# Kernel optimization log

Measured on AMD Instinct MI355X. Metric: run time of the kernel, lower is better.

Reference implementation:

```python
import jax, jax.numpy as jnp
import numpy as np

D_MODEL = 1024
NUM_HEADS = 16
HEAD_DIM = D_MODEL // NUM_HEADS
ROPE_BASE = 10000.0


def _rope_cos_sin(seq_len, head_dim, dtype):
    # inv_freq over half the head dim (standard 1D RoPE)
    inv_freq = 1.0 / (ROPE_BASE ** (jnp.arange(0, head_dim, 2, dtype=jnp.float32) / head_dim))
    ang = jnp.arange(seq_len, dtype=jnp.float32)[:, None] * inv_freq[None, :]  # [S, hd/2]
    cos = jnp.concatenate([jnp.cos(ang), jnp.cos(ang)], axis=-1).astype(dtype)  # [S, hd]
    sin = jnp.concatenate([jnp.sin(ang), jnp.sin(ang)], axis=-1).astype(dtype)
    return cos, sin


def _rotate_half(t):
    t1, t2 = jnp.split(t, 2, axis=-1)
    return jnp.concatenate([-t2, t1], axis=-1)


def _apply_rope(t, cos, sin):
    # t: [B, H, S, hd]; cos/sin: [S, hd]
    return t * cos[None, None, :, :] + _rotate_half(t) * sin[None, None, :, :]


def setup_inputs() -> dict:
    key = jax.random.key(0)
    k1, k2, k3 = jax.random.split(key, 3)
    B, S = 2, 2048
    x = jax.random.normal(k1, (B, S, D_MODEL), dtype=jnp.float32)
    w_qkv = jax.random.normal(k2, (D_MODEL, 3 * D_MODEL), dtype=jnp.float32) * (D_MODEL ** -0.5)
    w_proj = jax.random.normal(k3, (D_MODEL, D_MODEL), dtype=jnp.float32) * (D_MODEL ** -0.5)
    b_proj = jnp.zeros((D_MODEL,), dtype=jnp.float32)
    return {"x": x, "w_qkv": w_qkv, "w_proj": w_proj, "b_proj": b_proj, "causal": 1}


def reference(x, w_qkv, w_proj, b_proj, causal):
    B, S, D = x.shape
    scale = HEAD_DIM ** -0.5
    qkv = x @ w_qkv  # [B, S, 3D]
    q, k, v = jnp.split(qkv, 3, axis=-1)

    def to_heads(t):
        return t.reshape(B, S, NUM_HEADS, HEAD_DIM).transpose(0, 2, 1, 3)  # [B,H,S,hd]

    q, k, v = to_heads(q), to_heads(k), to_heads(v)

    cos, sin = _rope_cos_sin(S, HEAD_DIM, x.dtype)
    q = _apply_rope(q, cos, sin)
    k = _apply_rope(k, cos, sin)

    attn = jnp.einsum('bhqd,bhkd->bhqk', q, k) * scale  # [B,H,S,S]
    if causal:
        causal_mask = jnp.triu(jnp.ones((S, S), dtype=bool), k=1)
        attn = jnp.where(causal_mask[None, None, :, :], jnp.float32(-jnp.inf).astype(attn.dtype), attn)
    attn = jax.nn.softmax(attn, axis=-1)
    out = jnp.einsum('bhqk,bhkd->bhqd', attn, v)  # [B,H,S,hd]
    out = out.transpose(0, 2, 1, 3).reshape(B, S, D)
    return out @ w_proj + b_proj
```

## Files before the change

kernel.cpp:

```cpp
#include <hip/hip_runtime.h>
#include <stdint.h>
#include <math.h>

#define B_   2
#define S_   2048
#define D_   1024
#define H_   16
#define HD_  64
#define M_   (B_*S_)
#define N3_  (3*D_)

typedef __bf16 bf16;
typedef __bf16 bf16x2 __attribute__((ext_vector_type(2)));
typedef __bf16 bf16x4v __attribute__((ext_vector_type(4)));
typedef __bf16 bf16x8 __attribute__((ext_vector_type(8)));
typedef float  f32x4 __attribute__((ext_vector_type(4)));
typedef float  f32x16 __attribute__((ext_vector_type(16)));

__device__ __forceinline__ void gload_lds16(const void* g, void* l) {
  __builtin_amdgcn_global_load_lds(
      (__attribute__((address_space(1))) const unsigned int*)g,
      (__attribute__((address_space(3))) unsigned int*)l, 16, 0, 0);
}

__global__ __launch_bounds__(256) void prep_kernel(const float* __restrict__ x, bf16* __restrict__ xb,
                                                   const float* __restrict__ w_qkv, bf16* __restrict__ wqkvT,
                                                   const float* __restrict__ w_proj, bf16* __restrict__ wprojT,
                                                   float* __restrict__ cosT, float* __restrict__ sinT) {
  __shared__ float tile[32][33];
  int blk = blockIdx.x, tid = threadIdx.x;
  if (blk < 1024) {
#pragma unroll
    for (int it = 0; it < 4; it++) {
      int i = (blk * 4 + it) * 256 + tid;
      float4 v = ((const float4*)x)[i];
      bf16x4v o;
      o[0] = (bf16)v.x; o[1] = (bf16)v.y; o[2] = (bf16)v.z; o[3] = (bf16)v.w;
      *(bf16x4v*)(xb + (size_t)i * 4) = o;
    }
  } else if (blk < 5120) {
    const float* in; bf16* out; int R, C, tb;
    if (blk < 4096) { in = w_qkv;  out = wqkvT;  R = 1024; C = 3072; tb = blk - 1024; }
    else            { in = w_proj; out = wprojT; R = 1024; C = 1024; tb = blk - 4096; }
    int nbx = C >> 5;
    int bx = tb % nbx, by = tb / nbx;
    int c0 = bx * 32, r0 = by * 32;
    int tx = tid & 31, ty = tid >> 5;
#pragma unroll
    for (int j = 0; j < 4; j++)
      tile[ty + j * 8][tx] = in[(size_t)(r0 + ty + j * 8) * C + c0 + tx];
    __syncthreads();
#pragma unroll
    for (int j = 0; j < 4; j++)
      out[(size_t)(c0 + ty + j * 8) * R + r0 + tx] = (bf16)tile[tx][ty + j * 8];
  } else {
    int i = (blk - 5120) * 256 + tid;
    int s = i >> 5, d = i & 31;
    float inv = powf(10000.0f, -(float)d * (1.0f / 32.0f));
    float a = (float)s * inv;
    float sv, cv;
    sincosf(a, &sv, &cv);
    cosT[i] = cv; sinT[i] = sv;
  }
}

__global__ __launch_bounds__(256) void gemm128(const bf16* __restrict__ A,
                                               const bf16* __restrict__ Bt,
                                               int M, int N, int K,
                                               bf16* __restrict__ Cb,
                                               const float* __restrict__ cosT,
                                               const float* __restrict__ sinT,
                                               bf16* __restrict__ vt) {
  __shared__ bf16 As[128 * 32];
  __shared__ bf16 Bs[128 * 32];
  int tid = threadIdx.x;
  int lane = tid & 63, w = tid >> 6;
  int nwg = gridDim.x * gridDim.y;
  int bid = blockIdx.y * gridDim.x + blockIdx.x;
  int sw = (bid & 7) * (nwg >> 3) + (bid >> 3);
  int bx = sw % gridDim.x, by = sw / gridDim.x;
  int m0 = by * 128, n0 = bx * 128;
  int m_off = (w >> 1) * 64, n_off = (w & 1) * 64;
  f32x4 acc[4][4] = {};

  const char* Ab = (const char*)A;
  const char* Bb = (const char*)Bt;
  int srow = (lane >> 2);
  int skb  = (lane & 3) * 16;

  for (int k0 = 0; k0 < K; k0 += 32) {
    for (int j = 0; j < 2; j++) {
      int seg = j * 4 + w;
      int row = seg * 16 + srow;
      gload_lds16(Ab + ((size_t)(m0 + row) * K + k0) * 2 + skb, (char*)As + seg * 1024);
      gload_lds16(Bb + ((size_t)(n0 + row) * K + k0) * 2 + skb, (char*)Bs + seg * 1024);
    }
    __syncthreads();
    int rl = lane & 15;
    int kgb = (lane >> 4) * 16;
    bf16x8 a[4], b[4];
    for (int i = 0; i < 4; i++)
      a[i] = *(const bf16x8*)((const char*)As + (m_off + i * 16 + rl) * 64 + kgb);
    for (int i = 0; i < 4; i++)
      b[i] = *(const bf16x8*)((const char*)Bs + (n_off + i * 16 + rl) * 64 + kgb);
    for (int i = 0; i < 4; i++)
      for (int j = 0; j < 4; j++)
        acc[i][j] = __builtin_amdgcn_mfma_f32_16x16x32_bf16(a[i], b[j], acc[i][j], 0, 0, 0);
    __syncthreads();
  }

  int rq = (lane >> 4) * 4, cl = lane & 15;
  if ((n0 + n_off) < 2048) {
    for (int i = 0; i < 4; i++)
      for (int r = 0; r < 4; r++) {
        int row = m0 + m_off + i * 16 + rq + r;
        int srw = row & 2047;
        for (int j = 0; j < 2; j++) {
          int d2 = j * 16 + cl;
          float c = cosT[srw * 32 + d2], sn = sinT[srw * 32 + d2];
          float x1 = acc[i][j][r], x2 = acc[i][j + 2][r];
          Cb[(size_t)row * N + n0 + n_off + d2]      = (bf16)(x1 * c - x2 * sn);
          Cb[(size_t)row * N + n0 + n_off + d2 + 32] = (bf16)(x2 * c + x1 * sn);
        }
      }
  } else {
    int posbase = ((rq & 4) << 1) | ((rq & 8) >> 1);
    for (int i = 0; i < 4; i++) {
      int row0 = m0 + m_off + i * 16;
      int b = row0 >> 11;
      int sbase = (row0 & 2047) + posbase;
      for (int j = 0; j < 4; j++) {
        int col = n0 + n_off + j * 16 + cl - 2048;
        bf16x4v pv;
        pv[0] = (bf16)acc[i][j][0]; pv[1] = (bf16)acc[i][j][1];
        pv[2] = (bf16)acc[i][j][2]; pv[3] = (bf16)acc[i][j][3];
        *(bf16x4v*)(vt + ((size_t)(b * 1024 + col)) * 2048 + sbase) = pv;
      }
    }
  }
}

__global__ __launch_bounds__(256) void gemm_proj(const bf16* __restrict__ A,
                                                 const bf16* __restrict__ Bt,
                                                 float* __restrict__ Cf,
                                                 const float* __restrict__ bias) {
  __shared__ bf16 As[64 * 32];
  __shared__ bf16 Bs[128 * 32];
  const int K = 1024, N = 1024;
  int tid = threadIdx.x;
  int lane = tid & 63, w = tid >> 6;
  int bid = blockIdx.y * gridDim.x + blockIdx.x;
  int sw = (bid & 7) * 64 + (bid >> 3);
  int bx = sw & 7, by = sw >> 3;
  int m0 = by * 64, n0 = bx * 128;
  int m_off = (w >> 1) * 32, n_off = (w & 1) * 64;
  f32x4 acc[2][4] = {};

  const char* Ab = (const char*)A;
  const char* Bb = (const char*)Bt;
  int arow = tid >> 2, achk = (tid & 3) * 16;

  for (int k0 = 0; k0 < K; k0 += 32) {
    gload_lds16(Ab + ((size_t)(m0 + arow) * K + k0) * 2 + achk, (char*)As + tid * 16);
    gload_lds16(Bb + ((size_t)(n0 + arow) * K + k0) * 2 + achk, (char*)Bs + tid * 16);
    gload_lds16(Bb + ((size_t)(n0 + 64 + arow) * K + k0) * 2 + achk, (char*)Bs + 4096 + tid * 16);
    __syncthreads();
    int rl = lane & 15;
    int kgb = (lane >> 4) * 16;
    bf16x8 a[2], b[4];
    for (int i = 0; i < 2; i++)
      a[i] = *(const bf16x8*)((const char*)As + (m_off + i * 16 + rl) * 64 + kgb);
    for (int j = 0; j < 4; j++)
      b[j] = *(const bf16x8*)((const char*)Bs + (n_off + j * 16 + rl) * 64 + kgb);
    for (int i = 0; i < 2; i++)
      for (int j = 0; j < 4; j++)
        acc[i][j] = __builtin_amdgcn_mfma_f32_16x16x32_bf16(a[i], b[j], acc[i][j], 0, 0, 0);
    __syncthreads();
  }

  int rq = (lane >> 4) * 4, cl = lane & 15;
  for (int i = 0; i < 2; i++)
    for (int j = 0; j < 4; j++) {
      int col = n0 + n_off + j * 16 + cl;
      float bv = bias[col];
      for (int r = 0; r < 4; r++) {
        int row = m0 + m_off + i * 16 + rq + r;
        Cf[(size_t)row * N + col] = acc[i][j][r] + bv;
      }
    }
}

__global__ __launch_bounds__(512, 4) void attn_kernel(const bf16* __restrict__ qkv,
                                                      const bf16* __restrict__ vt,
                                                      bf16* __restrict__ O) {
  __shared__ __align__(16) unsigned char Ks[2][16384];
  __shared__ __align__(16) unsigned char Vs[2][16384];
  int tid = threadIdx.x, lane = tid & 63, w = tid >> 6;
  int qw = w & 3, p = w >> 2;
  int bid = blockIdx.x;
  int xcd = bid & 7, slot = bid >> 3;
  int bh = xcd * 4 + (slot & 3);
  int u = slot >> 2;
  int qt = 15 - u;
  int b = bh >> 4, h = bh & 15;
  int q0w = qt * 128 + qw * 32;
  int l31 = lane & 31, hi = lane >> 5;
  const char* qb = (const char*)qkv;
  const char* vb = (const char*)vt;

  int kr0 = tid >> 3, kcs = (tid & 7) ^ (kr0 & 7);
  int vr0 = tid >> 4, vcs = (tid & 15) ^ (vr0 & 7);

#define STAGE(buf, kvbase)                                                                              \
  do {                                                                                                  \
    gload_lds16(qb + (((size_t)(b * 2048 + (kvbase) + kr0) * 3072) + 1024 + h * 64) * 2 + kcs * 16,     \
                (char*)Ks[buf] + tid * 16);                                                             \
    gload_lds16(qb + (((size_t)(b * 2048 + (kvbase) + kr0 + 64) * 3072) + 1024 + h * 64) * 2 + kcs * 16,\
                (char*)Ks[buf] + (tid + 512) * 16);                                                     \
    gload_lds16(vb + (((size_t)(bh * 64 + vr0) * 2048) + (kvbase)) * 2 + vcs * 16,                      \
                (char*)Vs[buf] + tid * 16);                                                             \
    gload_lds16(vb + (((size_t)(bh * 64 + vr0 + 32) * 2048) + (kvbase)) * 2 + vcs * 16,                 \
                (char*)Vs[buf] + (tid + 512) * 16);                                                     \
  } while (0)

  bf16x8 aq[4];
#pragma unroll
  for (int s = 0; s < 4; s++) {
    size_t row = (size_t)(b * 2048 + q0w + l31);
    bf16x8 v = *(const bf16x8*)(qb + (row * 3072 + h * 64 + s * 16 + hi * 8) * 2);
#pragma unroll
    for (int e = 0; e < 8; e++) v[e] = (bf16)((float)v[e] * 0.18033688f);
    aq[s] = v;
  }

  f32x16 o0 = {}, o1 = {};
  float mrun = -3e38f, lrun = 0.f;
  int npair = qt + 1;

  STAGE(0, 0);
  asm volatile("s_waitcnt vmcnt(0)" ::: "memory");
  __builtin_amdgcn_s_barrier();

  for (int i = 0; i < npair; i++) {
    int cur = i & 1;
    if (i + 1 < npair) STAGE(cur ^ 1, (i + 1) * 128);

    int kvw = i * 128 + p * 64;
    if (kvw <= q0w + 31) {
      bool diag = (kvw + 63 > q0w);

      f32x16 scr[2];
#pragma unroll
      for (int kf = 0; kf < 2; kf++)
#pragma unroll
        for (int r = 0; r < 16; r++) scr[kf][r] = 0.f;
      __builtin_amdgcn_s_setprio(1);
#pragma unroll
      for (int s = 0; s < 4; s++) {
#pragma unroll
        for (int kf = 0; kf < 2; kf++) {
          int row = p * 64 + kf * 32 + l31;
          int ch = (hi + 2 * s) ^ (row & 7);
          bf16x8 ak = *(const bf16x8*)(Ks[cur] + row * 128 + ch * 16);
          scr[kf] = __builtin_amdgcn_mfma_f32_32x32x16_bf16(ak, aq[s], scr[kf], 0, 0, 0);
        }
      }
      __builtin_amdgcn_s_setprio(0);

      int qg = q0w + l31;
      if (diag) {
#pragma unroll
        for (int kf = 0; kf < 2; kf++)
#pragma unroll
          for (int r = 0; r < 16; r++) {
            int k = kvw + kf * 32 + (r & 3) + 8 * (r >> 2) + 4 * hi;
            if (k > qg) scr[kf][r] = -3e38f;
          }
      }

      float mx = -3e38f;
#pragma unroll
      for (int kf = 0; kf < 2; kf++)
#pragma unroll
        for (int r = 0; r < 16; r++) mx = fmaxf(mx, scr[kf][r]);
      mx = fmaxf(mx, __shfl_xor(mx, 32));

      if (!__all(mx - mrun <= 11.5f)) {
        float mnew = fmaxf(mrun, mx);
        float corr = exp2f(mrun - mnew);
        mrun = mnew;
        lrun *= corr;
#pragma unroll
        for (int r = 0; r < 16; r++) {
          float cr = __shfl(corr, (r & 3) + 8 * (r >> 2) + 4 * hi);
          o0[r] *= cr; o1[r] *= cr;
        }
      }

      float rs = 0.f;
      unsigned D[2][8];
#pragma unroll
      for (int kf = 0; kf < 2; kf++)
#pragma unroll
        for (int j = 0; j < 8; j++) {
          float p0 = exp2f(scr[kf][2 * j] - mrun);
          float p1 = exp2f(scr[kf][2 * j + 1] - mrun);
          rs += p0 + p1;
          bf16x2 tp; tp[0] = (bf16)p0; tp[1] = (bf16)p1;
          D[kf][j] = __builtin_bit_cast(unsigned, tp);
        }
      rs += __shfl_xor(rs, 32);
      lrun += rs;

#pragma unroll
      for (int kf = 0; kf < 2; kf++) {
#pragma unroll
        for (int sg = 0; sg < 2; sg++) {
          union { unsigned u4[4]; bf16x8 v; } ap;
          ap.u4[0] = D[kf][4 * sg + 0];
          ap.u4[1] = D[kf][4 * sg + 1];
          ap.u4[2] = D[kf][4 * sg + 2];
          ap.u4[3] = D[kf][4 * sg + 3];
          __builtin_amdgcn_s_setprio(1);
#pragma unroll
          for (int nf = 0; nf < 2; nf++) {
            int row = nf * 32 + l31;
            int ch = ((p * 8) + (hi + 2 * sg + 4 * kf)) ^ (row & 7);
            bf16x8 bv = *(const bf16x8*)(Vs[cur] + row * 256 + ch * 16);
            if (nf == 0) o0 = __builtin_amdgcn_mfma_f32_32x32x16_bf16(ap.v, bv, o0, 0, 0, 0);
            else         o1 = __builtin_amdgcn_mfma_f32_32x32x16_bf16(ap.v, bv, o1, 0, 0, 0);
          }
          __builtin_amdgcn_s_setprio(0);
        }
      }
    }

    asm volatile("s_waitcnt vmcnt(0)" ::: "memory");
    __builtin_amdgcn_s_barrier();
  }

  float* mlb = (float*)Ks;
  if (hi == 0) {
    mlb[((qw * 2 + p) * 2 + 0) * 32 + l31] = mrun;
    mlb[((qw * 2 + p) * 2 + 1) * 32 + l31] = lrun;
  }
  __syncthreads();
  float m_o = mlb[((qw * 2 + (1 - p)) * 2 + 0) * 32 + l31];
  float l_o = mlb[((qw * 2 + (1 - p)) * 2 + 1) * 32 + l31];
  float Mm = fmaxf(mrun, m_o);
  float cs = exp2f(mrun - Mm);
  float L  = lrun * cs + l_o * exp2f(m_o - Mm);
  float* obuf = (float*)Vs;
  if (p == 1) {
#pragma unroll
    for (int r = 0; r < 16; r++) {
      int crow = (r & 3) + 8 * (r >> 2) + 4 * hi;
      float c = __shfl(cs, crow);
      obuf[qw * 2048 + r * 64 + lane]        = o0[r] * c;
      obuf[qw * 2048 + (r + 16) * 64 + lane] = o1[r] * c;
    }
  }
  __syncthreads();
  if (p == 0) {
    float linv = 1.0f / L;
#pragma unroll
    for (int r = 0; r < 16; r++) {
      int crow = (r & 3) + 8 * (r >> 2) + 4 * hi;
      float c  = __shfl(cs, crow);
      float li = __shfl(linv, crow);
      size_t row = (size_t)(b * 2048 + q0w + crow);
      float v0 = (o0[r] * c + obuf[qw * 2048 + r * 64 + lane]) * li;
      float v1 = (o1[r] * c + obuf[qw * 2048 + (r + 16) * 64 + lane]) * li;
      O[row * 1024 + h * 64 + l31]      = (bf16)v0;
      O[row * 1024 + h * 64 + 32 + l31] = (bf16)v1;
    }
  }
#undef STAGE
}

extern "C" void kernel_launch(void* const* d_in, const int* in_sizes, int n_in,
                              void* d_out, int out_size, void* d_ws, size_t ws_size,
                              hipStream_t stream) {
  const float* x      = (const float*)d_in[0];
  const float* w_qkv  = (const float*)d_in[1];
  const float* w_proj = (const float*)d_in[2];
  const float* b_proj = (const float*)d_in[3];

  char* ws = (char*)d_ws;
  size_t off = 0;
  bf16* xb     = (bf16*)(ws + off); off += (size_t)M_ * D_ * 2;
  bf16* wqkvT  = (bf16*)(ws + off); off += (size_t)N3_ * D_ * 2;
  bf16* wprojT = (bf16*)(ws + off); off += (size_t)D_ * D_ * 2;
  bf16* qkvb   = (bf16*)(ws + off); off += (size_t)M_ * N3_ * 2;
  bf16* ob     = (bf16*)(ws + off); off += (size_t)M_ * D_ * 2;
  bf16* vtb    = (bf16*)(ws + off); off += (size_t)M_ * D_ * 2;
  float* cosT  = (float*)(ws + off); off += (size_t)S_ * 32 * 4;
  float* sinT  = (float*)(ws + off); off += (size_t)S_ * 32 * 4;

  prep_kernel<<<5376, 256, 0, stream>>>(x, xb, w_qkv, wqkvT, w_proj, wprojT, cosT, sinT);
  gemm128<<<dim3(N3_ / 128, M_ / 128), 256, 0, stream>>>(xb, wqkvT, M_, N3_, D_, qkvb, cosT, sinT, vtb);
  attn_kernel<<<512, 512, 0, stream>>>(qkvb, vtb, ob);
  gemm_proj<<<dim3(8, 64), 256, 0, stream>>>(ob, wprojT, (float*)d_out, b_proj);
}
```

Baseline: 113.5 us.

## Rewrite QKV GEMM with 128x192 double-buffered swizzled tiles; widen proj K-step; fast exp2

The QKV GEMM becomes 512-thread blocks with 128x192 tiles (three heads per block), K-step 64 and double-buffered LDS staging that overlaps the next tile load with the MFMAs. LDS uses an XOR chunk swizzle to avoid bank conflicts. The projection GEMM gets the same swizzle and a doubled K-step to halve barriers, and the attention softmax switches to the hardware exp2 intrinsic. The cost is higher LDS use per block (80KB), which may limit occupancy, and slightly less accurate exp2.

```diff
diff --git a/kernel.cpp b/kernel.cpp
--- a/kernel.cpp
+++ b/kernel.cpp
@@ -21,6 +21,10 @@
   __builtin_amdgcn_global_load_lds(
       (__attribute__((address_space(1))) const unsigned int*)g,
       (__attribute__((address_space(3))) unsigned int*)l, 16, 0, 0);
+}
+
+__device__ __forceinline__ float fast_exp2(float x) {
+  return __builtin_amdgcn_exp2f(x);
 }
 
 __global__ __launch_bounds__(256) void prep_kernel(const float* __restrict__ x, bf16* __restrict__ xb,
@@ -64,88 +68,114 @@
   }
 }
 
-__global__ __launch_bounds__(256) void gemm128(const bf16* __restrict__ A,
-                                               const bf16* __restrict__ Bt,
-                                               int M, int N, int K,
-                                               bf16* __restrict__ Cb,
-                                               const float* __restrict__ cosT,
-                                               const float* __restrict__ sinT,
-                                               bf16* __restrict__ vt) {
-  __shared__ bf16 As[128 * 32];
-  __shared__ bf16 Bs[128 * 32];
-  int tid = threadIdx.x;
-  int lane = tid & 63, w = tid >> 6;
-  int nwg = gridDim.x * gridDim.y;
+__global__ __launch_bounds__(512, 4) void gemm_qkv(const bf16* __restrict__ A,
+                                                   const bf16* __restrict__ Bt,
+                                                   bf16* __restrict__ Cb,
+                                                   const float* __restrict__ cosT,
+                                                   const float* __restrict__ sinT,
+                                                   bf16* __restrict__ vt) {
+  __shared__ __align__(16) unsigned char lds[81920];
+  const int K = 1024;
+  int tid = threadIdx.x, lane = tid & 63, w = tid >> 6;
   int bid = blockIdx.y * gridDim.x + blockIdx.x;
-  int sw = (bid & 7) * (nwg >> 3) + (bid >> 3);
-  int bx = sw % gridDim.x, by = sw / gridDim.x;
-  int m0 = by * 128, n0 = bx * 128;
-  int m_off = (w >> 1) * 64, n_off = (w & 1) * 64;
-  f32x4 acc[4][4] = {};
-
+  int sw = (bid & 7) * 64 + (bid >> 3);
+  int bx = sw & 15, by = sw >> 4;
+  int m0 = by * 128, n0 = bx * 192;
+  int rl = lane & 15, kg = lane >> 4;
+
+  int r8 = tid >> 3;
+  int cSw = ((tid & 7) ^ (r8 & 7)) * 16;
   const char* Ab = (const char*)A;
   const char* Bb = (const char*)Bt;
-  int srow = (lane >> 2);
-  int skb  = (lane & 3) * 16;
-
-  for (int k0 = 0; k0 < K; k0 += 32) {
-    for (int j = 0; j < 2; j++) {
-      int seg = j * 4 + w;
-      int row = seg * 16 + srow;
-      gload_lds16(Ab + ((size_t)(m0 + row) * K + k0) * 2 + skb, (char*)As + seg * 1024);
-      gload_lds16(Bb + ((size_t)(n0 + row) * K + k0) * 2 + skb, (char*)Bs + seg * 1024);
-    }
-    __syncthreads();
-    int rl = lane & 15;
-    int kgb = (lane >> 4) * 16;
-    bf16x8 a[4], b[4];
-    for (int i = 0; i < 4; i++)
-      a[i] = *(const bf16x8*)((const char*)As + (m_off + i * 16 + rl) * 64 + kgb);
-    for (int i = 0; i < 4; i++)
-      b[i] = *(const bf16x8*)((const char*)Bs + (n_off + i * 16 + rl) * 64 + kgb);
-    for (int i = 0; i < 4; i++)
-      for (int j = 0; j < 4; j++)
-        acc[i][j] = __builtin_amdgcn_mfma_f32_16x16x32_bf16(a[i], b[j], acc[i][j], 0, 0, 0);
-    __syncthreads();
-  }
-
-  int rq = (lane >> 4) * 4, cl = lane & 15;
-  if ((n0 + n_off) < 2048) {
-    for (int i = 0; i < 4; i++)
-      for (int r = 0; r < 4; r++) {
-        int row = m0 + m_off + i * 16 + rq + r;
-        int srw = row & 2047;
-        for (int j = 0; j < 2; j++) {
-          int d2 = j * 16 + cl;
+
+#define QSTG(kt, bf)                                                                        \
+  do {                                                                                      \
+    char* base = (char*)lds + (bf) * 40960;                                                 \
+    _Pragma("unroll")                                                                       \
+    for (int s = 0; s < 2; s++)                                                             \
+      gload_lds16(Ab + ((size_t)(m0 + s * 64 + r8) * K + (kt) * 64) * 2 + cSw,              \
+                  base + s * 8192 + tid * 16);                                              \
+    _Pragma("unroll")                                                                       \
+    for (int s = 0; s < 3; s++)                                                             \
+      gload_lds16(Bb + ((size_t)(n0 + s * 64 + r8) * K + (kt) * 64) * 2 + cSw,              \
+                  base + 16384 + s * 8192 + tid * 16);                                      \
+  } while (0)
+
+  int ch0 = ((kg + 0) ^ (rl & 7)) * 16;
+  int ch1 = ((kg + 4) ^ (rl & 7)) * 16;
+  int aoff = (w * 16 + rl) * 128;
+
+  f32x4 acc[12] = {};
+
+  QSTG(0, 0);
+  asm volatile("s_waitcnt vmcnt(0)" ::: "memory");
+  __builtin_amdgcn_s_barrier();
+
+  for (int kt = 0; kt < 16; kt++) {
+    int cur = kt & 1;
+    if (kt + 1 < 16) QSTG(kt + 1, cur ^ 1);
+    const char* base = (const char*)lds + cur * 40960;
+    bf16x8 a0 = *(const bf16x8*)(base + aoff + ch0);
+    bf16x8 a1 = *(const bf16x8*)(base + aoff + ch1);
+    __builtin_amdgcn_s_setprio(1);
+#pragma unroll
+    for (int br = 0; br < 12; br++) {
+      int boff = 16384 + (br * 16 + rl) * 128;
+      bf16x8 b0 = *(const bf16x8*)(base + boff + ch0);
+      bf16x8 b1 = *(const bf16x8*)(base + boff + ch1);
+      acc[br] = __builtin_amdgcn_mfma_f32_16x16x32_bf16(a0, b0, acc[br], 0, 0, 0);
+      acc[br] = __builtin_amdgcn_mfma_f32_16x16x32_bf16(a1, b1, acc[br], 0, 0, 0);
+    }
+    __builtin_amdgcn_s_setprio(0);
+    asm volatile("s_waitcnt vmcnt(0)" ::: "memory");
+    __builtin_amdgcn_s_barrier();
+  }
+
+  int rq = kg * 4;
+#pragma unroll
+  for (int hb = 0; hb < 3; hb++) {
+    int g0 = n0 + hb * 64;
+    if (g0 < 2048) {
+#pragma unroll
+      for (int j = 0; j < 2; j++) {
+        int br = hb * 4 + j;
+#pragma unroll
+        for (int r = 0; r < 4; r++) {
+          int row = m0 + w * 16 + rq + r;
+          int srw = row & 2047;
+          int d2 = j * 16 + rl;
           float c = cosT[srw * 32 + d2], sn = sinT[srw * 32 + d2];
-          float x1 = acc[i][j][r], x2 = acc[i][j + 2][r];
-          Cb[(size_t)row * N + n0 + n_off + d2]      = (bf16)(x1 * c - x2 * sn);
-          Cb[(size_t)row * N + n0 + n_off + d2 + 32] = (bf16)(x2 * c + x1 * sn);
+          float x1 = acc[br][r], x2 = acc[br + 2][r];
+          size_t o = (size_t)row * 3072 + g0 + d2;
+          Cb[o]      = (bf16)(x1 * c - x2 * sn);
+          Cb[o + 32] = (bf16)(x2 * c + x1 * sn);
         }
       }
-  } else {
-    int posbase = ((rq & 4) << 1) | ((rq & 8) >> 1);
-    for (int i = 0; i < 4; i++) {
-      int row0 = m0 + m_off + i * 16;
-      int b = row0 >> 11;
+    } else {
+      int posbase = ((rq & 4) << 1) | ((rq & 8) >> 1);
+      int row0 = m0 + w * 16;
+      int bb = row0 >> 11;
       int sbase = (row0 & 2047) + posbase;
+#pragma unroll
       for (int j = 0; j < 4; j++) {
-        int col = n0 + n_off + j * 16 + cl - 2048;
+        int br = hb * 4 + j;
+        int col = g0 + j * 16 + rl - 2048;
         bf16x4v pv;
-        pv[0] = (bf16)acc[i][j][0]; pv[1] = (bf16)acc[i][j][1];
-        pv[2] = (bf16)acc[i][j][2]; pv[3] = (bf16)acc[i][j][3];
-        *(bf16x4v*)(vt + ((size_t)(b * 1024 + col)) * 2048 + sbase) = pv;
-      }
-    }
-  }
+        pv[0] = (bf16)acc[br][0]; pv[1] = (bf16)acc[br][1];
+        pv[2] = (bf16)acc[br][2]; pv[3] = (bf16)acc[br][3];
+        *(bf16x4v*)(vt + ((size_t)(bb * 1024 + col)) * 2048 + sbase) = pv;
+      }
+    }
+  }
+#undef QSTG
 }
 
 __global__ __launch_bounds__(256) void gemm_proj(const bf16* __restrict__ A,
                                                  const bf16* __restrict__ Bt,
                                                  float* __restrict__ Cf,
                                                  const float* __restrict__ bias) {
-  __shared__ bf16 As[64 * 32];
-  __shared__ bf16 Bs[128 * 32];
+  __shared__ __align__(16) unsigned char As[8192];
+  __shared__ __align__(16) unsigned char Bs[16384];
   const int K = 1024, N = 1024;
   int tid = threadIdx.x;
   int lane = tid & 63, w = tid >> 6;
@@ -154,34 +184,58 @@
   int bx = sw & 7, by = sw >> 3;
   int m0 = by * 64, n0 = bx * 128;
   int m_off = (w >> 1) * 32, n_off = (w & 1) * 64;
+  int rl = lane & 15, kg = lane >> 4;
   f32x4 acc[2][4] = {};
 
   const char* Ab = (const char*)A;
   const char* Bb = (const char*)Bt;
-  int arow = tid >> 2, achk = (tid & 3) * 16;
-
-  for (int k0 = 0; k0 < K; k0 += 32) {
-    gload_lds16(Ab + ((size_t)(m0 + arow) * K + k0) * 2 + achk, (char*)As + tid * 16);
-    gload_lds16(Bb + ((size_t)(n0 + arow) * K + k0) * 2 + achk, (char*)Bs + tid * 16);
-    gload_lds16(Bb + ((size_t)(n0 + 64 + arow) * K + k0) * 2 + achk, (char*)Bs + 4096 + tid * 16);
+  int r8 = tid >> 3;
+  int cSw = ((tid & 7) ^ (r8 & 7)) * 16;
+
+  int ch0 = ((0 + kg) ^ (rl & 7)) * 16;
+  int ch1 = ((4 + kg) ^ (rl & 7)) * 16;
+
+  for (int k0 = 0; k0 < K; k0 += 64) {
+#pragma unroll
+    for (int s = 0; s < 2; s++) {
+      int row = s * 32 + r8;
+      gload_lds16(Ab + ((size_t)(m0 + row) * K + k0) * 2 + cSw, (char*)As + s * 4096 + tid * 16);
+    }
+#pragma unroll
+    for (int s = 0; s < 4; s++) {
+      int row = s * 32 + r8;
+      gload_lds16(Bb + ((size_t)(n0 + row) * K + k0) * 2 + cSw, (char*)Bs + s * 4096 + tid * 16);
+    }
     __syncthreads();
-    int rl = lane & 15;
-    int kgb = (lane >> 4) * 16;
-    bf16x8 a[2], b[4];
+    bf16x8 a[2][2], b[4][2];
+#pragma unroll
+    for (int i = 0; i < 2; i++) {
+      int row = m_off + i * 16 + rl;
+      a[i][0] = *(const bf16x8*)((const char*)As + row * 128 + ch0);
+      a[i][1] = *(const bf16x8*)((const char*)As + row * 128 + ch1);
+    }
+#pragma unroll
+    for (int j = 0; j < 4; j++) {
+      int row = n_off + j * 16 + rl;
+      b[j][0] = *(const bf16x8*)((const char*)Bs + row * 128 + ch0);
+      b[j][1] = *(const bf16x8*)((const char*)Bs + row * 128 + ch1);
+    }
+    __builtin_amdgcn_s_setprio(1);
+#pragma unroll
     for (int i = 0; i < 2; i++)
-      a[i] = *(const bf16x8*)((const char*)As + (m_off + i * 16 + rl) * 64 + kgb);
-    for (int j = 0; j < 4; j++)
-      b[j] = *(const bf16x8*)((const char*)Bs + (n_off + j * 16 + rl) * 64 + kgb);
-    for (int i = 0; i < 2; i++)
-      for (int j = 0; j < 4; j++)
-        acc[i][j] = __builtin_amdgcn_mfma_f32_16x16x32_bf16(a[i], b[j], acc[i][j], 0, 0, 0);
+#pragma unroll
+      for (int j = 0; j < 4; j++) {
+        acc[i][j] = __builtin_amdgcn_mfma_f32_16x16x32_bf16(a[i][0], b[j][0], acc[i][j], 0, 0, 0);
+        acc[i][j] = __builtin_amdgcn_mfma_f32_16x16x32_bf16(a[i][1], b[j][1], acc[i][j], 0, 0, 0);
+      }
+    __builtin_amdgcn_s_setprio(0);
     __syncthreads();
   }
 
-  int rq = (lane >> 4) * 4, cl = lane & 15;
+  int rq = kg * 4;
   for (int i = 0; i < 2; i++)
     for (int j = 0; j < 4; j++) {
-      int col = n0 + n_off + j * 16 + cl;
+      int col = n0 + n_off + j * 16 + rl;
       float bv = bias[col];
       for (int r = 0; r < 4; r++) {
         int row = m0 + m_off + i * 16 + rq + r;
@@ -303,8 +357,8 @@
       for (int kf = 0; kf < 2; kf++)
 #pragma unroll
         for (int j = 0; j < 8; j++) {
-          float p0 = exp2f(scr[kf][2 * j] - mrun);
-          float p1 = exp2f(scr[kf][2 * j + 1] - mrun);
+          float p0 = fast_exp2(scr[kf][2 * j] - mrun);
+          float p1 = fast_exp2(scr[kf][2 * j + 1] - mrun);
           rs += p0 + p1;
           bf16x2 tp; tp[0] = (bf16)p0; tp[1] = (bf16)p1;
           D[kf][j] = __builtin_bit_cast(unsigned, tp);
@@ -398,7 +452,7 @@
   float* sinT  = (float*)(ws + off); off += (size_t)S_ * 32 * 4;
 
   prep_kernel<<<5376, 256, 0, stream>>>(x, xb, w_qkv, wqkvT, w_proj, wprojT, cosT, sinT);
-  gemm128<<<dim3(N3_ / 128, M_ / 128), 256, 0, stream>>>(xb, wqkvT, M_, N3_, D_, qkvb, cosT, sinT, vtb);
+  gemm_qkv<<<dim3(16, 32), 512, 0, stream>>>(xb, wqkvT, qkvb, cosT, sinT, vtb);
   attn_kernel<<<512, 512, 0, stream>>>(qkvb, vtb, ob);
   gemm_proj<<<dim3(8, 64), 256, 0, stream>>>(ob, wprojT, (float*)d_out, b_proj);
 }
```

After: 96.77 us (median of 2 runs). 14.7% less time.
